# Optimization experiments

Hardware: AMD Instinct MI355X
Metric: run time of the kernel (lower is better)

The kernel has to match this reference:

```python
import jax, jax.numpy as jnp
import numpy as np

NUM_HEADS = 8
WS = 8  # window size


def setup_inputs() -> dict:
    key = jax.random.key(0)
    k1, k2, k3 = jax.random.split(key, 3)
    C = 384
    x = jax.random.normal(k1, (2, C, 256, 256), dtype=jnp.float32)
    # Conv2d 1x1 weights squeezed to [out_ch, in_ch]
    w_qkv = jax.random.normal(k2, (3 * C, C), dtype=jnp.float32) * 0.02
    w_proj = jax.random.normal(k3, (C, C), dtype=jnp.float32) * 0.02
    return {"x": x, "w_qkv": w_qkv, "w_proj": w_proj}


def reference(x, w_qkv, w_proj):
    b, c, h, w = x.shape
    ws = WS
    nh = NUM_HEADS
    hd = c // nh
    scale = hd ** -0.5
    pad_h = (ws - h % ws) % ws
    pad_w = (ws - w % ws) % ws
    if pad_h or pad_w:  # static shapes -> Python if is jit-safe
        x = jnp.pad(x, ((0, 0), (0, 0), (0, pad_h), (0, pad_w)), mode='reflect')
    hp, wp = x.shape[2], x.shape[3]

    # 1x1 conv == channel GEMM
    qkv = jnp.einsum('bchw,oc->bohw', x, w_qkv)  # [b, 3c, hp, wp]
    q, k, v = jnp.split(qkv, 3, axis=1)

    def window_partition(t):
        # [b,c,hp,wp] -> [b*nWindows, nh, ws*ws, hd]
        t = t.reshape(b, nh, hd, hp // ws, ws, wp // ws, ws)
        t = t.transpose(0, 3, 5, 1, 4, 6, 2)
        return t.reshape(-1, nh, ws * ws, hd)

    qw = window_partition(q)
    kw = window_partition(k)
    vw = window_partition(v)

    attn = jax.nn.softmax(jnp.einsum('wnqd,wnkd->wnqk', qw, kw) * scale, axis=-1)
    out = jnp.einsum('wnqk,wnkd->wnqd', attn, vw)

    # merge windows back to [b, c, hp, wp]
    out = out.reshape(b, hp // ws, wp // ws, nh, ws, ws, hd)
    out = out.transpose(0, 3, 6, 1, 4, 2, 5).reshape(b, c, hp, wp)

    out = jnp.einsum('bchw,oc->bohw', out, w_proj)
    if pad_h or pad_w:
        out = out[:, :, :h, :w]
    return out
```

## Files before the change

### kernel.cpp

```cpp
#include <hip/hip_runtime.h>


#define NPIX 131072
#define KDIM 384
#define SCALE 0.14433756729740643f

typedef __attribute__((ext_vector_type(8))) short bf16x8;
typedef __attribute__((ext_vector_type(4))) float floatx4;

__device__ __forceinline__ unsigned short f2b(float f) {
  union { float f; unsigned u; } v; v.f = f;
  return (unsigned short)((v.u + 0x7FFFu + ((v.u >> 16) & 1u)) >> 16);
}

__device__ __forceinline__ floatx4 mfma_bf16(bf16x8 a, bf16x8 b, floatx4 c) {
  return __builtin_amdgcn_mfma_f32_16x16x32_bf16(a, b, c, 0, 0, 0);
}

__device__ __forceinline__ void async16(const void* g, void* lds) {
  __builtin_amdgcn_global_load_lds(
      (const __attribute__((address_space(1))) unsigned int*)g,
      (__attribute__((address_space(3))) unsigned int*)lds, 16, 0, 0);
}

__global__ __launch_bounds__(256) void wcvt(const float* __restrict__ wq,
                                            const float* __restrict__ wp,
                                            unsigned short* __restrict__ wqb,
                                            unsigned short* __restrict__ wpb) {
  int i = blockIdx.x * 256 + threadIdx.x;
  if (i < 1152 * 384) wqb[i] = f2b(wq[i]);
  if (i < 384 * 384)  wpb[i] = f2b(wp[i]);
}

__global__ __launch_bounds__(256) void transpose_cast(const float* __restrict__ x,
                                                      unsigned short* __restrict__ xT) {
  __shared__ unsigned short sT[256 * 40];
  int id = blockIdx.x;
  int cg = id % 12; id /= 12;
  int wxg = id % 8; id /= 8;
  int wy = id % 32; id /= 32;
  int b = id;
  int tid = threadIdx.x;
  const float* xb = x + ((size_t)(b * 384 + cg * 32)) * 65536 + (size_t)(wy * 8) * 256 + wxg * 32;
#pragma unroll
  for (int it = 0; it < 8; ++it) {
    int e = it * 256 + tid;
    int c = e >> 6, rem = e & 63, y = rem >> 3, x4 = rem & 7;
    float4 v = *(const float4*)&xb[(size_t)c * 65536 + y * 256 + x4 * 4];
    int xx = x4 * 4;
    int p0 = (xx >> 3) * 64 + y * 8 + (xx & 7);
    unsigned short* dst = &sT[p0 * 40 + c];
    dst[0]   = f2b(v.x);
    dst[40]  = f2b(v.y);
    dst[80]  = f2b(v.z);
    dst[120] = f2b(v.w);
  }
  __syncthreads();
  int wl = tid >> 6, t = tid & 63;
  size_t pix = (size_t)b * 65536 + (size_t)(wy * 32 + wxg * 4 + wl) * 64 + t;
  unsigned short* dst = xT + pix * 384 + cg * 32;
  const unsigned short* src = &sT[tid * 40];
#pragma unroll
  for (int q = 0; q < 4; ++q)
    *(uint4*)(dst + q * 8) = *(const uint4*)(src + q * 8);
}

template <int MODE>
__global__ __launch_bounds__(256, 2) void gemm_bt(const unsigned short* __restrict__ A,
                                                  const unsigned short* __restrict__ B,
                                                  void* __restrict__ Cout,
                                                  int M, int N, int K) {
  __shared__ uint4 smem4[2176];
  unsigned short* As = (unsigned short*)smem4;
  unsigned short* Bs = (unsigned short*)smem4 + 128 * 64;
  const int tid = threadIdx.x;
  const int MT = M >> 7;

  const int per = gridDim.x >> 3;
  const int vbid = (blockIdx.x & 7) * per + (blockIdx.x >> 3);
  const int Mbase = (vbid % MT) * 128;
  const int Nbase = (vbid / MT) * 128;

  const int wave = tid >> 6, lane = tid & 63;
  const int wm = wave >> 1, wn = wave & 1;
  const int l16 = lane & 15, quad = lane >> 4;
  const int Kv = K >> 3;
  const int kTiles = K >> 6;

  const int lr = lane >> 3;
  const int kbs = (lane & 7) ^ lr;
  const int mrow = wave * 8 + lr;

  floatx4 acc[4][4];
#pragma unroll
  for (int mt = 0; mt < 4; ++mt)
#pragma unroll
    for (int nt = 0; nt < 4; ++nt) acc[mt][nt] = 0.f;

  const uint4* Ag = (const uint4*)(A + (size_t)Mbase * K);
  const uint4* Bg = (const uint4*)(B + (size_t)Nbase * K);

  for (int kt = 0; kt < kTiles; ++kt) {
    __syncthreads();
#pragma unroll
    for (int j = 0; j < 4; ++j) {
      int m = j * 32 + mrow;
      async16(Ag + (size_t)m * Kv + kt * 8 + kbs, (char*)As + j * 4096 + wave * 1024);
      async16(Bg + (size_t)m * Kv + kt * 8 + kbs, (char*)Bs + j * 4096 + wave * 1024);
    }
    __syncthreads();
#pragma unroll
    for (int s = 0; s < 2; ++s) {
      bf16x8 af[4], bfr[4];
#pragma unroll
      for (int mt = 0; mt < 4; ++mt) {
        int m = wm * 64 + mt * 16 + l16;
        int kk = (s * 4 + quad) ^ (m & 7);
        af[mt] = *(const bf16x8*)&As[(m * 8 + kk) * 8];
      }
#pragma unroll
      for (int nt = 0; nt < 4; ++nt) {
        int n = wn * 64 + nt * 16 + l16;
        int kk = (s * 4 + quad) ^ (n & 7);
        bfr[nt] = *(const bf16x8*)&Bs[(n * 8 + kk) * 8];
      }
#pragma unroll
      for (int mt = 0; mt < 4; ++mt)
#pragma unroll
        for (int nt = 0; nt < 4; ++nt)
          acc[mt][nt] = mfma_bf16(af[mt], bfr[nt], acc[mt][nt]);
    }
  }

  if (MODE == 0) {
    unsigned short* Cs = (unsigned short*)smem4;
    __syncthreads();
#pragma unroll
    for (int mt = 0; mt < 4; ++mt)
#pragma unroll
      for (int nt = 0; nt < 4; ++nt)
#pragma unroll
        for (int r = 0; r < 4; ++r) {
          int lm = wm * 64 + mt * 16 + quad * 4 + r;
          int ln = wn * 64 + nt * 16 + l16;
          Cs[lm * 136 + ln] = f2b(acc[mt][nt][r]);
        }
    __syncthreads();
#pragma unroll
    for (int it = 0; it < 8; ++it) {
      int slot = it * 256 + tid;
      int row = slot >> 4, ch = slot & 15;
      *(uint4*)((unsigned short*)Cout + (size_t)(Mbase + row) * N + Nbase + ch * 8) =
          *(const uint4*)&Cs[row * 136 + ch * 8];
    }
  } else {
    float* Fs = (float*)smem4;
    const int b = Nbase >> 16;
    const int win0 = (Nbase & 65535) >> 6;
    const int hh0 = (win0 >> 5) * 8;
    const int ww0 = (win0 & 31) * 8;
#pragma unroll
    for (int p = 0; p < 2; ++p) {
      __syncthreads();
#pragma unroll
      for (int mth = 0; mth < 2; ++mth) {
        int mt = p * 2 + mth;
#pragma unroll
        for (int nt = 0; nt < 4; ++nt)
#pragma unroll
          for (int r = 0; r < 4; ++r) {
            int lrow = wm * 32 + mth * 16 + quad * 4 + r;
            int ln = wn * 64 + nt * 16 + l16;
            Fs[lrow * 136 + ln] = acc[mt][nt][r];
          }
      }
      __syncthreads();
#pragma unroll
      for (int it = 0; it < 8; ++it) {
        int slot = it * 256 + tid;
        int q4 = slot & 3;
        int seg = slot >> 2;
        int ty = seg & 7, lrow = seg >> 3;
        int m = Mbase + (lrow >> 5) * 64 + p * 32 + (lrow & 31);
        int base_col = (q4 >> 1) * 64 + ty * 8 + (q4 & 1) * 4;
        float4 v = *(const float4*)&Fs[lrow * 136 + base_col];
        float* dst = (float*)Cout + ((size_t)(b * 384 + m)) * 65536 +
                     (size_t)(hh0 + ty) * 256 + ww0 + q4 * 4;
        *(float4*)dst = v;
      }
    }
  }
}

__global__ __launch_bounds__(256, 2) void attn_kernel(const unsigned short* __restrict__ qkv,
                                                      unsigned short* __restrict__ ao) {
  __shared__ unsigned short sQ[64 * 72];
  __shared__ unsigned short sK[64 * 72];
  __shared__ unsigned short sV[48 * 72];
  __shared__ unsigned short sP[64 * 72];
  const int wh = blockIdx.x;
  const int wing = wh >> 3, h = wh & 7;
  const int wb = wing * 64;
  const int tid = threadIdx.x;

  {
    if (tid < 128) {
      int t = tid >> 1, ch = tid & 1;
      const uint4 z = {0u, 0u, 0u, 0u};
      *(uint4*)&sQ[t * 72 + 48 + ch * 8] = z;
      *(uint4*)&sK[t * 72 + 48 + ch * 8] = z;
    }
#pragma unroll
    for (int j = 0; j < 3; ++j) {
      int task = j * 256 + tid;
      int d = task >> 4, g = task & 15;
      uint2 vq = *(const uint2*)&qkv[(size_t)(h * 48 + d) * NPIX + wb + g * 4];
      uint2 vk = *(const uint2*)&qkv[(size_t)(384 + h * 48 + d) * NPIX + wb + g * 4];
      unsigned short* q0 = &sQ[(g * 4) * 72 + d];
      unsigned short* k0 = &sK[(g * 4) * 72 + d];
      q0[0]   = (unsigned short)(vq.x);
      q0[72]  = (unsigned short)(vq.x >> 16);
      q0[144] = (unsigned short)(vq.y);
      q0[216] = (unsigned short)(vq.y >> 16);
      k0[0]   = (unsigned short)(vk.x);
      k0[72]  = (unsigned short)(vk.x >> 16);
      k0[144] = (unsigned short)(vk.y);
      k0[216] = (unsigned short)(vk.y >> 16);
    }
    for (int idx = tid; idx < 384; idx += 256) {
      int d = idx >> 3, c8 = idx & 7;
      *(uint4*)&sV[d * 72 + c8 * 8] =
          *(const uint4*)&qkv[(size_t)(768 + h * 48 + d) * NPIX + wb + c8 * 8];
    }
  }
  __syncthreads();

  const int wave = tid >> 6, lane = tid & 63;
  const int l16 = lane & 15, quad = lane >> 4;
  const int tb = wave * 16;

  floatx4 sacc[4];
#pragma unroll
  for (int nt = 0; nt < 4; ++nt) sacc[nt] = 0.f;
#pragma unroll
  for (int s = 0; s < 2; ++s) {
    bf16x8 aq = *(const bf16x8*)&sQ[(tb + l16) * 72 + s * 32 + quad * 8];
#pragma unroll
    for (int nt = 0; nt < 4; ++nt) {
      bf16x8 bk = *(const bf16x8*)&sK[(nt * 16 + l16) * 72 + s * 32 + quad * 8];
      sacc[nt] = mfma_bf16(aq, bk, sacc[nt]);
    }
  }
#pragma unroll
  for (int r = 0; r < 4; ++r) {
    float v0 = sacc[0][r] * SCALE, v1 = sacc[1][r] * SCALE;
    float v2 = sacc[2][r] * SCALE, v3 = sacc[3][r] * SCALE;
    float mx = fmaxf(fmaxf(v0, v1), fmaxf(v2, v3));
    mx = fmaxf(mx, __shfl_xor(mx, 1));
    mx = fmaxf(mx, __shfl_xor(mx, 2));
    mx = fmaxf(mx, __shfl_xor(mx, 4));
    mx = fmaxf(mx, __shfl_xor(mx, 8));
    float p0 = __expf(v0 - mx), p1 = __expf(v1 - mx);
    float p2 = __expf(v2 - mx), p3 = __expf(v3 - mx);
    float sum = p0 + p1 + p2 + p3;
    sum += __shfl_xor(sum, 1);
    sum += __shfl_xor(sum, 2);
    sum += __shfl_xor(sum, 4);
    sum += __shfl_xor(sum, 8);
    float inv = 1.f / sum;
    int t = tb + quad * 4 + r;
    sP[t * 72 + 0 * 16 + l16] = f2b(p0 * inv);
    sP[t * 72 + 1 * 16 + l16] = f2b(p1 * inv);
    sP[t * 72 + 2 * 16 + l16] = f2b(p2 * inv);
    sP[t * 72 + 3 * 16 + l16] = f2b(p3 * inv);
  }
  __syncthreads();

  floatx4 oacc[3];
#pragma unroll
  for (int nt = 0; nt < 3; ++nt) oacc[nt] = 0.f;
#pragma unroll
  for (int s = 0; s < 2; ++s) {
    bf16x8 ap = *(const bf16x8*)&sP[(tb + l16) * 72 + s * 32 + quad * 8];
#pragma unroll
    for (int nt = 0; nt < 3; ++nt) {
      bf16x8 bv = *(const bf16x8*)&sV[(nt * 16 + l16) * 72 + s * 32 + quad * 8];
      oacc[nt] = mfma_bf16(ap, bv, oacc[nt]);
    }
  }
#pragma unroll
  for (int nt = 0; nt < 3; ++nt) {
#pragma unroll
    for (int r = 0; r < 4; ++r) {
      int t = tb + quad * 4 + r;
      int d = nt * 16 + l16;
      ao[((size_t)(wb + t)) * 384 + h * 48 + d] = f2b(oacc[nt][r]);
    }
  }
}

extern "C" void kernel_launch(void* const* d_in, const int* in_sizes, int n_in,
                              void* d_out, int out_size, void* d_ws, size_t ws_size,
                              hipStream_t stream) {
  const float* x  = (const float*)d_in[0];
  const float* wq = (const float*)d_in[1];
  const float* wp = (const float*)d_in[2];
  float* out = (float*)d_out;

  char* ws = (char*)d_ws;
  unsigned short* xT  = (unsigned short*)(ws);
  unsigned short* qkv = (unsigned short*)(ws + 100663296ull);
  unsigned short* ao  = (unsigned short*)(ws + 402653184ull);
  unsigned short* wqb = (unsigned short*)(ws + 503316480ull);
  unsigned short* wpb = (unsigned short*)(ws + 504201216ull);

  wcvt<<<1728, 256, 0, stream>>>(wq, wp, wqb, wpb);
  transpose_cast<<<6144, 256, 0, stream>>>(x, xT);
  gemm_bt<0><<<9216, 256, 0, stream>>>(wqb, xT, qkv, 1152, NPIX, KDIM);
  attn_kernel<<<16384, 256, 0, stream>>>(qkv, ao);
  gemm_bt<1><<<3072, 256, 0, stream>>>(wpb, ao, out, 384, NPIX, KDIM);
}
```

Measured before the change: 740.0 us.

## Fuse window attention with output projection and store QKV window-major

```diff
diff --git a/kernel.cpp b/kernel.cpp
--- a/kernel.cpp
+++ b/kernel.cpp
@@ -65,11 +65,10 @@
     *(uint4*)(dst + q * 8) = *(const uint4*)(src + q * 8);
 }
 
-template <int MODE>
-__global__ __launch_bounds__(256, 2) void gemm_bt(const unsigned short* __restrict__ A,
-                                                  const unsigned short* __restrict__ B,
-                                                  void* __restrict__ Cout,
-                                                  int M, int N, int K) {
+__global__ __launch_bounds__(256, 4) void gemm_qkv(const unsigned short* __restrict__ A,
+                                                   const unsigned short* __restrict__ B,
+                                                   unsigned short* __restrict__ qkv2,
+                                                   int M, int N, int K) {
   __shared__ uint4 smem4[2176];
   unsigned short* As = (unsigned short*)smem4;
   unsigned short* Bs = (unsigned short*)smem4 + 128 * 64;
@@ -132,171 +131,192 @@
     }
   }
 
-  if (MODE == 0) {
-    unsigned short* Cs = (unsigned short*)smem4;
-    __syncthreads();
-#pragma unroll
-    for (int mt = 0; mt < 4; ++mt)
-#pragma unroll
-      for (int nt = 0; nt < 4; ++nt)
-#pragma unroll
-        for (int r = 0; r < 4; ++r) {
-          int lm = wm * 64 + mt * 16 + quad * 4 + r;
-          int ln = wn * 64 + nt * 16 + l16;
-          Cs[lm * 136 + ln] = f2b(acc[mt][nt][r]);
-        }
-    __syncthreads();
-#pragma unroll
-    for (int it = 0; it < 8; ++it) {
-      int slot = it * 256 + tid;
-      int row = slot >> 4, ch = slot & 15;
-      *(uint4*)((unsigned short*)Cout + (size_t)(Mbase + row) * N + Nbase + ch * 8) =
-          *(const uint4*)&Cs[row * 136 + ch * 8];
-    }
-  } else {
-    float* Fs = (float*)smem4;
-    const int b = Nbase >> 16;
-    const int win0 = (Nbase & 65535) >> 6;
-    const int hh0 = (win0 >> 5) * 8;
-    const int ww0 = (win0 & 31) * 8;
-#pragma unroll
-    for (int p = 0; p < 2; ++p) {
-      __syncthreads();
-#pragma unroll
-      for (int mth = 0; mth < 2; ++mth) {
-        int mt = p * 2 + mth;
-#pragma unroll
-        for (int nt = 0; nt < 4; ++nt)
-#pragma unroll
-          for (int r = 0; r < 4; ++r) {
-            int lrow = wm * 32 + mth * 16 + quad * 4 + r;
-            int ln = wn * 64 + nt * 16 + l16;
-            Fs[lrow * 136 + ln] = acc[mt][nt][r];
-          }
-      }
-      __syncthreads();
-#pragma unroll
-      for (int it = 0; it < 8; ++it) {
-        int slot = it * 256 + tid;
-        int q4 = slot & 3;
-        int seg = slot >> 2;
-        int ty = seg & 7, lrow = seg >> 3;
-        int m = Mbase + (lrow >> 5) * 64 + p * 32 + (lrow & 31);
-        int base_col = (q4 >> 1) * 64 + ty * 8 + (q4 & 1) * 4;
-        float4 v = *(const float4*)&Fs[lrow * 136 + base_col];
-        float* dst = (float*)Cout + ((size_t)(b * 384 + m)) * 65536 +
-                     (size_t)(hh0 + ty) * 256 + ww0 + q4 * 4;
-        *(float4*)dst = v;
-      }
-    }
-  }
-}
-
-__global__ __launch_bounds__(256, 2) void attn_kernel(const unsigned short* __restrict__ qkv,
-                                                      unsigned short* __restrict__ ao) {
+  unsigned short* Cs = (unsigned short*)smem4;
+  __syncthreads();
+#pragma unroll
+  for (int mt = 0; mt < 4; ++mt)
+#pragma unroll
+    for (int nt = 0; nt < 4; ++nt)
+#pragma unroll
+      for (int r = 0; r < 4; ++r) {
+        int lm = wm * 64 + mt * 16 + quad * 4 + r;
+        int ln = wn * 64 + nt * 16 + l16;
+        Cs[lm * 136 + ln] = f2b(acc[mt][nt][r]);
+      }
+  __syncthreads();
+  const int wing0 = Nbase >> 6;
+#pragma unroll
+  for (int it = 0; it < 8; ++it) {
+    int slot = it * 256 + tid;
+    int row = slot >> 4, ch = slot & 15;
+    unsigned short* dst = qkv2 + (size_t)(wing0 + (ch >> 3)) * 73728 +
+                          (size_t)(Mbase + row) * 64 + (ch & 7) * 8;
+    *(uint4*)dst = *(const uint4*)&Cs[row * 136 + ch * 8];
+  }
+}
+
+__global__ __launch_bounds__(256, 2) void attnproj(const unsigned short* __restrict__ qkv2,
+                                                   const unsigned short* __restrict__ wpb,
+                                                   float* __restrict__ out) {
+  __shared__ unsigned short sAOT[64 * 392];
   __shared__ unsigned short sQ[64 * 72];
   __shared__ unsigned short sK[64 * 72];
   __shared__ unsigned short sV[48 * 72];
-  __shared__ unsigned short sP[64 * 72];
-  const int wh = blockIdx.x;
-  const int wing = wh >> 3, h = wh & 7;
-  const int wb = wing * 64;
+
+  const int bid = blockIdx.x;
+  const int wing = (bid & 7) * 256 + (bid >> 3);
+  const int b = wing >> 10, win = wing & 1023;
+  const int hh0 = (win >> 5) * 8, ww0 = (win & 31) * 8;
   const int tid = threadIdx.x;
-
-  {
-    if (tid < 128) {
-      int t = tid >> 1, ch = tid & 1;
-      const uint4 z = {0u, 0u, 0u, 0u};
-      *(uint4*)&sQ[t * 72 + 48 + ch * 8] = z;
-      *(uint4*)&sK[t * 72 + 48 + ch * 8] = z;
-    }
-#pragma unroll
-    for (int j = 0; j < 3; ++j) {
-      int task = j * 256 + tid;
-      int d = task >> 4, g = task & 15;
-      uint2 vq = *(const uint2*)&qkv[(size_t)(h * 48 + d) * NPIX + wb + g * 4];
-      uint2 vk = *(const uint2*)&qkv[(size_t)(384 + h * 48 + d) * NPIX + wb + g * 4];
-      unsigned short* q0 = &sQ[(g * 4) * 72 + d];
-      unsigned short* k0 = &sK[(g * 4) * 72 + d];
-      q0[0]   = (unsigned short)(vq.x);
-      q0[72]  = (unsigned short)(vq.x >> 16);
-      q0[144] = (unsigned short)(vq.y);
-      q0[216] = (unsigned short)(vq.y >> 16);
-      k0[0]   = (unsigned short)(vk.x);
-      k0[72]  = (unsigned short)(vk.x >> 16);
-      k0[144] = (unsigned short)(vk.y);
-      k0[216] = (unsigned short)(vk.y >> 16);
-    }
-    for (int idx = tid; idx < 384; idx += 256) {
-      int d = idx >> 3, c8 = idx & 7;
-      *(uint4*)&sV[d * 72 + c8 * 8] =
-          *(const uint4*)&qkv[(size_t)(768 + h * 48 + d) * NPIX + wb + c8 * 8];
-    }
-  }
-  __syncthreads();
+  const unsigned short* base = qkv2 + (size_t)wing * 73728;
 
   const int wave = tid >> 6, lane = tid & 63;
   const int l16 = lane & 15, quad = lane >> 4;
   const int tb = wave * 16;
 
-  floatx4 sacc[4];
-#pragma unroll
-  for (int nt = 0; nt < 4; ++nt) sacc[nt] = 0.f;
-#pragma unroll
-  for (int s = 0; s < 2; ++s) {
-    bf16x8 aq = *(const bf16x8*)&sQ[(tb + l16) * 72 + s * 32 + quad * 8];
-#pragma unroll
-    for (int nt = 0; nt < 4; ++nt) {
-      bf16x8 bk = *(const bf16x8*)&sK[(nt * 16 + l16) * 72 + s * 32 + quad * 8];
-      sacc[nt] = mfma_bf16(aq, bk, sacc[nt]);
-    }
-  }
-#pragma unroll
-  for (int r = 0; r < 4; ++r) {
-    float v0 = sacc[0][r] * SCALE, v1 = sacc[1][r] * SCALE;
-    float v2 = sacc[2][r] * SCALE, v3 = sacc[3][r] * SCALE;
-    float mx = fmaxf(fmaxf(v0, v1), fmaxf(v2, v3));
-    mx = fmaxf(mx, __shfl_xor(mx, 1));
-    mx = fmaxf(mx, __shfl_xor(mx, 2));
-    mx = fmaxf(mx, __shfl_xor(mx, 4));
-    mx = fmaxf(mx, __shfl_xor(mx, 8));
-    float p0 = __expf(v0 - mx), p1 = __expf(v1 - mx);
-    float p2 = __expf(v2 - mx), p3 = __expf(v3 - mx);
-    float sum = p0 + p1 + p2 + p3;
-    sum += __shfl_xor(sum, 1);
-    sum += __shfl_xor(sum, 2);
-    sum += __shfl_xor(sum, 4);
-    sum += __shfl_xor(sum, 8);
-    float inv = 1.f / sum;
-    int t = tb + quad * 4 + r;
-    sP[t * 72 + 0 * 16 + l16] = f2b(p0 * inv);
-    sP[t * 72 + 1 * 16 + l16] = f2b(p1 * inv);
-    sP[t * 72 + 2 * 16 + l16] = f2b(p2 * inv);
-    sP[t * 72 + 3 * 16 + l16] = f2b(p3 * inv);
-  }
+  if (tid < 64) {
+    const uint4 z = {0u, 0u, 0u, 0u};
+    *(uint4*)&sK[tid * 72 + 48] = z;
+    *(uint4*)&sK[tid * 72 + 56] = z;
+    *(uint4*)&sQ[tid * 72 + 48] = z;
+    *(uint4*)&sQ[tid * 72 + 56] = z;
+  }
+
+  int qd[3], qg[3], qko[3];
+#pragma unroll
+  for (int j = 0; j < 3; ++j) {
+    int task = j * 256 + tid;
+    int isK = task >= 384;
+    int r = task - (isK ? 384 : 0);
+    qd[j] = r >> 3; qg[j] = r & 7; qko[j] = isK ? 24576 : 0;
+  }
+  const int vd0 = tid >> 3, vc8 = tid & 7;
+
+  uint4 vqk[3], vv0, vv1;
+#pragma unroll
+  for (int j = 0; j < 3; ++j)
+    vqk[j] = *(const uint4*)(base + qko[j] + qd[j] * 64 + qg[j] * 8);
+  vv0 = *(const uint4*)(base + 49152 + vd0 * 64 + vc8 * 8);
+  if (tid < 128) vv1 = *(const uint4*)(base + 49152 + (32 + vd0) * 64 + vc8 * 8);
+
+#pragma unroll
+  for (int h = 0; h < 8; ++h) {
+    __syncthreads();
+#pragma unroll
+    for (int j = 0; j < 3; ++j) {
+      unsigned short* dst = (qko[j] ? sK : sQ) + (qg[j] * 8) * 72 + qd[j];
+      uint4 v = vqk[j];
+      dst[0]   = (unsigned short)(v.x);
+      dst[72]  = (unsigned short)(v.x >> 16);
+      dst[144] = (unsigned short)(v.y);
+      dst[216] = (unsigned short)(v.y >> 16);
+      dst[288] = (unsigned short)(v.z);
+      dst[360] = (unsigned short)(v.z >> 16);
+      dst[432] = (unsigned short)(v.w);
+      dst[504] = (unsigned short)(v.w >> 16);
+    }
+    *(uint4*)&sV[vd0 * 72 + vc8 * 8] = vv0;
+    if (tid < 128) *(uint4*)&sV[(32 + vd0) * 72 + vc8 * 8] = vv1;
+    if (h < 7) {
+      int hb = (h + 1) * 48;
+#pragma unroll
+      for (int j = 0; j < 3; ++j)
+        vqk[j] = *(const uint4*)(base + qko[j] + (hb + qd[j]) * 64 + qg[j] * 8);
+      vv0 = *(const uint4*)(base + 49152 + (hb + vd0) * 64 + vc8 * 8);
+      if (tid < 128) vv1 = *(const uint4*)(base + 49152 + (hb + 32 + vd0) * 64 + vc8 * 8);
+    }
+    __syncthreads();
+
+    floatx4 sacc[4];
+#pragma unroll
+    for (int nt = 0; nt < 4; ++nt) sacc[nt] = 0.f;
+#pragma unroll
+    for (int s = 0; s < 2; ++s) {
+      bf16x8 aq = *(const bf16x8*)&sQ[(tb + l16) * 72 + s * 32 + quad * 8];
+#pragma unroll
+      for (int nt = 0; nt < 4; ++nt) {
+        bf16x8 bk = *(const bf16x8*)&sK[(nt * 16 + l16) * 72 + s * 32 + quad * 8];
+        sacc[nt] = mfma_bf16(aq, bk, sacc[nt]);
+      }
+    }
+    unsigned short* sP = sQ;
+#pragma unroll
+    for (int r = 0; r < 4; ++r) {
+      float v0 = sacc[0][r] * SCALE, v1 = sacc[1][r] * SCALE;
+      float v2 = sacc[2][r] * SCALE, v3 = sacc[3][r] * SCALE;
+      float mx = fmaxf(fmaxf(v0, v1), fmaxf(v2, v3));
+      mx = fmaxf(mx, __shfl_xor(mx, 1));
+      mx = fmaxf(mx, __shfl_xor(mx, 2));
+      mx = fmaxf(mx, __shfl_xor(mx, 4));
+      mx = fmaxf(mx, __shfl_xor(mx, 8));
+      float p0 = __expf(v0 - mx), p1 = __expf(v1 - mx);
+      float p2 = __expf(v2 - mx), p3 = __expf(v3 - mx);
+      float sum = p0 + p1 + p2 + p3;
+      sum += __shfl_xor(sum, 1);
+      sum += __shfl_xor(sum, 2);
+      sum += __shfl_xor(sum, 4);
+      sum += __shfl_xor(sum, 8);
+      float inv = 1.f / sum;
+      int t = tb + quad * 4 + r;
+      sP[t * 72 + 0 * 16 + l16] = f2b(p0 * inv);
+      sP[t * 72 + 1 * 16 + l16] = f2b(p1 * inv);
+      sP[t * 72 + 2 * 16 + l16] = f2b(p2 * inv);
+      sP[t * 72 + 3 * 16 + l16] = f2b(p3 * inv);
+    }
+    floatx4 oacc[3];
+#pragma unroll
+    for (int nt = 0; nt < 3; ++nt) oacc[nt] = 0.f;
+#pragma unroll
+    for (int s = 0; s < 2; ++s) {
+      bf16x8 ap = *(const bf16x8*)&sP[(tb + l16) * 72 + s * 32 + quad * 8];
+#pragma unroll
+      for (int nt = 0; nt < 3; ++nt) {
+        bf16x8 bv = *(const bf16x8*)&sV[(nt * 16 + l16) * 72 + s * 32 + quad * 8];
+        oacc[nt] = mfma_bf16(ap, bv, oacc[nt]);
+      }
+    }
+#pragma unroll
+    for (int nt = 0; nt < 3; ++nt)
+#pragma unroll
+      for (int r = 0; r < 4; ++r) {
+        int t = tb + quad * 4 + r, d = nt * 16 + l16;
+        sAOT[t * 392 + h * 48 + d] = f2b(oacc[nt][r]);
+      }
+  }
+
   __syncthreads();
 
-  floatx4 oacc[3];
-#pragma unroll
-  for (int nt = 0; nt < 3; ++nt) oacc[nt] = 0.f;
-#pragma unroll
-  for (int s = 0; s < 2; ++s) {
-    bf16x8 ap = *(const bf16x8*)&sP[(tb + l16) * 72 + s * 32 + quad * 8];
-#pragma unroll
-    for (int nt = 0; nt < 3; ++nt) {
-      bf16x8 bv = *(const bf16x8*)&sV[(nt * 16 + l16) * 72 + s * 32 + quad * 8];
-      oacc[nt] = mfma_bf16(ap, bv, oacc[nt]);
-    }
-  }
-#pragma unroll
-  for (int nt = 0; nt < 3; ++nt) {
-#pragma unroll
-    for (int r = 0; r < 4; ++r) {
-      int t = tb + quad * 4 + r;
-      int d = nt * 16 + l16;
-      ao[((size_t)(wb + t)) * 384 + h * 48 + d] = f2b(oacc[nt][r]);
-    }
-  }
+  floatx4 pacc[6][4];
+#pragma unroll
+  for (int mt = 0; mt < 6; ++mt)
+#pragma unroll
+    for (int nt = 0; nt < 4; ++nt) pacc[mt][nt] = 0.f;
+  const int o0 = wave * 96;
+#pragma unroll
+  for (int kc = 0; kc < 12; ++kc) {
+    bf16x8 bfp[4];
+#pragma unroll
+    for (int nt = 0; nt < 4; ++nt)
+      bfp[nt] = *(const bf16x8*)&sAOT[(nt * 16 + l16) * 392 + kc * 32 + quad * 8];
+#pragma unroll
+    for (int mt = 0; mt < 6; ++mt) {
+      bf16x8 af = *(const bf16x8*)&wpb[(size_t)(o0 + mt * 16 + l16) * 384 + kc * 32 + quad * 8];
+#pragma unroll
+      for (int nt = 0; nt < 4; ++nt)
+        pacc[mt][nt] = mfma_bf16(af, bfp[nt], pacc[mt][nt]);
+    }
+  }
+  float* outb = out + (size_t)b * 384 * 65536 + (size_t)hh0 * 256 + ww0;
+#pragma unroll
+  for (int mt = 0; mt < 6; ++mt)
+#pragma unroll
+    for (int nt = 0; nt < 4; ++nt)
+#pragma unroll
+      for (int r = 0; r < 4; ++r) {
+        int o = o0 + mt * 16 + quad * 4 + r;
+        int t = nt * 16 + l16;
+        outb[(size_t)o * 65536 + (t >> 3) * 256 + (t & 7)] = pacc[mt][nt][r];
+      }
 }
 
 extern "C" void kernel_launch(void* const* d_in, const int* in_sizes, int n_in,
@@ -308,15 +328,13 @@
   float* out = (float*)d_out;
 
   char* ws = (char*)d_ws;
-  unsigned short* xT  = (unsigned short*)(ws);
-  unsigned short* qkv = (unsigned short*)(ws + 100663296ull);
-  unsigned short* ao  = (unsigned short*)(ws + 402653184ull);
-  unsigned short* wqb = (unsigned short*)(ws + 503316480ull);
-  unsigned short* wpb = (unsigned short*)(ws + 504201216ull);
+  unsigned short* xT   = (unsigned short*)(ws);
+  unsigned short* qkv2 = (unsigned short*)(ws + 100663296ull);
+  unsigned short* wqb  = (unsigned short*)(ws + 402653184ull);
+  unsigned short* wpb  = (unsigned short*)(ws + 403537920ull);
 
   wcvt<<<1728, 256, 0, stream>>>(wq, wp, wqb, wpb);
   transpose_cast<<<6144, 256, 0, stream>>>(x, xT);
-  gemm_bt<0><<<9216, 256, 0, stream>>>(wqb, xT, qkv, 1152, NPIX, KDIM);
-  attn_kernel<<<16384, 256, 0, stream>>>(qkv, ao);
-  gemm_bt<1><<<3072, 256, 0, stream>>>(wpb, ao, out, 384, NPIX, KDIM);
-}
+  gemm_qkv<<<9216, 256, 0, stream>>>(wqb, xT, qkv2, 1152, NPIX, KDIM);
+  attnproj<<<2048, 256, 0, stream>>>(qkv2, wpb, out);
+}
```

After: 711.9 us. 1.04x faster.
